# Performance work log

Hardware: AMD Instinct MI355X
Metric: run time of the kernel (lower is better)

## Reference

```python
import jax, jax.numpy as jnp
import numpy as np

HIDDEN = 2048
N_HEADS = 16
N_KV_HEADS = 8
HEAD_DIM = 128  # == head_dim_original, no padding needed
ROPE_THETA = 1000000.0
EPS = 1e-6
T_NOISE = 512
T_CTX = 1536
MAX_KV = 8192


def rms_norm(x, scale, eps=EPS):
    # normalize over last axis (head_dim), per-head like nnx.RMSNorm(head_dim)
    var = jnp.mean(x * x, axis=-1, keepdims=True)
    return x * jax.lax.rsqrt(var + eps) * scale


def apply_rope(x, positions, head_dim=HEAD_DIM, theta=ROPE_THETA):
    # x: (T, N, H), positions: (T,) int
    inv_freq = 1.0 / (theta ** (jnp.arange(0, head_dim, 2, dtype=jnp.float32) / head_dim))
    ang = positions.astype(jnp.float32)[:, None] * inv_freq  # (T, H/2)
    cos = jnp.cos(ang)[:, None, :]  # (T, 1, H/2)
    sin = jnp.sin(ang)[:, None, :]
    x1, x2 = jnp.split(x, 2, axis=-1)
    return jnp.concatenate([x1 * cos - x2 * sin, x2 * cos + x1 * sin], axis=-1).astype(x.dtype)


def setup_inputs() -> dict:
    key = jax.random.key(0)
    ks = jax.random.split(key, 10)
    s = 0.02
    return {
        "x_noise": jax.random.normal(ks[0], (T_NOISE, HIDDEN), jnp.float32),
        "target_hidden": jax.random.normal(ks[1], (T_CTX, HIDDEN), jnp.float32),
        "noise_positions": jnp.arange(T_NOISE, dtype=jnp.int32) + T_CTX,
        "ctx_positions": jnp.arange(T_CTX, dtype=jnp.int32),
        "kv_cache_k": jax.random.normal(ks[2], (1, N_HEADS, MAX_KV, HEAD_DIM), jnp.float32),
        "kv_cache_v": jax.random.normal(ks[3], (1, N_HEADS, MAX_KV, HEAD_DIM), jnp.float32),
        "cache_len": 2048,
        "wq": jax.random.normal(ks[4], (HIDDEN, N_HEADS, HEAD_DIM), jnp.float32) * s,
        "wk": jax.random.normal(ks[5], (HIDDEN, N_KV_HEADS, HEAD_DIM), jnp.float32) * s,
        "wv": jax.random.normal(ks[6], (HIDDEN, N_KV_HEADS, HEAD_DIM), jnp.float32) * s,
        "wo": jax.random.normal(ks[7], (N_HEADS, HEAD_DIM, HIDDEN), jnp.float32) * s,
        "q_scale": jnp.ones((HEAD_DIM,), jnp.float32) + jax.random.uniform(ks[8], (HEAD_DIM,), jnp.float32, -0.05, 0.05),
        "k_scale": jnp.ones((HEAD_DIM,), jnp.float32) + jax.random.uniform(ks[9], (HEAD_DIM,), jnp.float32, -0.05, 0.05),
    }


def reference(x_noise, target_hidden, noise_positions, ctx_positions, kv_cache_k,
              kv_cache_v, cache_len, wq, wk, wv, wo, q_scale, k_scale):
    num_kv_groups = N_HEADS // N_KV_HEADS
    t_noise = x_noise.shape[0]

    # 1. Q projection + RMSNorm + RoPE
    q = jnp.einsum('td,dnh->tnh', x_noise, wq)
    q = rms_norm(q, q_scale)
    q = apply_rope(q, noise_positions)

    # 2. K/V over [context, noise]
    x_new = jnp.concatenate([target_hidden, x_noise], axis=0)  # (T_new, D)
    k_new = jnp.einsum('td,dkh->tkh', x_new, wk)
    v_new = jnp.einsum('td,dkh->tkh', x_new, wv)
    k_new = rms_norm(k_new, k_scale)
    new_positions = jnp.concatenate([ctx_positions, noise_positions], axis=0)
    k_new = apply_rope(k_new, new_positions)

    # 3. GQA head repeat
    if num_kv_groups > 1:
        k_new = jnp.repeat(k_new, num_kv_groups, axis=1)
        v_new = jnp.repeat(v_new, num_kv_groups, axis=1)

    # 4. Scatter new K/V into cache at dynamic offset cache_len
    t_new = x_new.shape[0]
    k_new_4d = k_new.transpose(1, 0, 2)[None]  # (1, N, T_new, H)
    v_new_4d = v_new.transpose(1, 0, 2)[None]
    kv_cache_k = jax.lax.dynamic_update_slice(kv_cache_k, k_new_4d, (0, 0, cache_len, 0))
    kv_cache_v = jax.lax.dynamic_update_slice(kv_cache_v, v_new_4d, (0, 0, cache_len, 0))
    new_cache_len = cache_len + t_new
    max_kv = kv_cache_k.shape[2]

    # 5. Non-causal attention over valid cache (segment-id mask = valid length)
    q_4d = q.transpose(1, 0, 2)[None]  # (1, N, T_noise, H)
    sm_scale = HEAD_DIM ** -0.5
    scores = jnp.einsum('bnth,bnsh->bnts', q_4d, kv_cache_k) * sm_scale  # (1,N,Tq,S)
    valid = jnp.arange(max_kv) < new_cache_len  # (S,)
    scores = jnp.where(valid[None, None, None, :], scores, jnp.float32(-1e30))
    probs = jax.nn.softmax(scores, axis=-1)
    attn = jnp.einsum('bnts,bnsh->bnth', probs, kv_cache_v)
    attn = attn[0].transpose(1, 0, 2)  # (T_noise, N, H)

    output = jnp.einsum('tnh,nhd->td', attn, wo)
    return output, kv_cache_k, kv_cache_v
```

## Files before the change

### kernel.cpp

```cpp
#include <hip/hip_runtime.h>
#include <hip/hip_bf16.h>

#define HIDDEN 2048
#define NH 16
#define NKV 8
#define HD 128
#define TN 512
#define TC 1536
#define TNEW 2048
#define MAXKV 8192

using u16 = unsigned short;
using u32 = unsigned int;

typedef short short8 __attribute__((ext_vector_type(8)));
typedef float floatx4 __attribute__((ext_vector_type(4)));

__device__ __forceinline__ u16 f2bf(float f) {
  u32 u = __float_as_uint(f);
  u += 0x7FFFu + ((u >> 16) & 1u);
  return (u16)(u >> 16);
}

__device__ __forceinline__ uint4 pack8(const float* f) {
  uint4 r;
  r.x = (u32)f2bf(f[0]) | ((u32)f2bf(f[1]) << 16);
  r.y = (u32)f2bf(f[2]) | ((u32)f2bf(f[3]) << 16);
  r.z = (u32)f2bf(f[4]) | ((u32)f2bf(f[5]) << 16);
  r.w = (u32)f2bf(f[6]) | ((u32)f2bf(f[7]) << 16);
  return r;
}

__device__ __forceinline__ short8 ldfrag(const u16* p) {
  uint4 v = *(const uint4*)p;
  return __builtin_bit_cast(short8, v);
}

__device__ __forceinline__ void gload16(const void* g, void* l) {
  __builtin_amdgcn_global_load_lds(
      (const __attribute__((address_space(1))) u32*)g,
      (__attribute__((address_space(3))) u32*)l, 16, 0, 0);
}

__global__ __launch_bounds__(256) void cache_copy(
    const float4* __restrict__ inK, const float4* __restrict__ inV,
    float4* __restrict__ outK, float4* __restrict__ outV,
    const int* __restrict__ clp, u16* __restrict__ Kb, u16* __restrict__ VbT)
{
  const int cl = *clp;
  long long idx = (long long)blockIdx.x * 256 + threadIdx.x;
  const long long per = (long long)NH * MAXKV * (HD / 4);
  const float4* src; float4* dst; bool isv;
  long long r = idx;
  if (r < per) { src = inK; dst = outK; isv = false; }
  else { r -= per; src = inV; dst = outV; isv = true; }
  int row = (int)((r >> 5) & (MAXKV - 1));
  if (row >= cl && row < cl + TNEW) return;
  float4 v = src[r];
  dst[r] = v;
  if (row < cl) {
    if (!isv) {
      if (Kb) {
        uint2 p;
        p.x = (u32)f2bf(v.x) | ((u32)f2bf(v.y) << 16);
        p.y = (u32)f2bf(v.z) | ((u32)f2bf(v.w) << 16);
        *(uint2*)(Kb + (size_t)r * 4) = p;
      }
    } else if (VbT) {
      int head = (int)(r >> 18);
      int h0 = ((int)r & 31) * 4;
      size_t basev = ((size_t)head * HD + h0) * MAXKV + row;
      VbT[basev]             = f2bf(v.x);
      VbT[basev + MAXKV]     = f2bf(v.y);
      VbT[basev + 2 * MAXKV] = f2bf(v.z);
      VbT[basev + 3 * MAXKV] = f2bf(v.w);
    }
  }
}

__global__ __launch_bounds__(256) void gemm_bf16(
    const float* __restrict__ A0, int rows0, const float* __restrict__ A1,
    const float* __restrict__ B0, const float* __restrict__ B1, int Nhalf,
    float* __restrict__ C0, float* __restrict__ C1,
    int M, int N, int K, int ksteps)
{
  __shared__ u16 As[64 * 40];
  __shared__ u16 Bs[64 * 40];
  const int tid = threadIdx.x;
  const int lane = tid & 63;
  const int wave = tid >> 6;
  const int quad = lane >> 4;
  const int m16 = lane & 15;
  const int bm = blockIdx.y * 64;
  const int bn = blockIdx.x * 64;
  const int wm = (wave >> 1) * 32;
  const int wn = (wave & 1) * 32;
  const int z = blockIdx.z;
  const int kbase = z * ksteps * 32;

  const float* B = (bn < Nhalf) ? B0 : B1;
  float*       C = (bn < Nhalf) ? C0 : C1;
  const int n0 = (bn < Nhalf) ? bn : bn - Nhalf;
  const int strideN = (bn < Nhalf) ? Nhalf : (N - Nhalf);

  floatx4 acc[2][2];
#pragma unroll
  for (int i = 0; i < 2; i++)
#pragma unroll
    for (int j = 0; j < 2; j++)
#pragma unroll
      for (int r = 0; r < 4; r++) acc[i][j][r] = 0.0f;

  const int arow = tid >> 2, akg = (tid & 3) * 8;
  const int brow = tid >> 3, bng = (tid & 7) * 8;
  const int garow = bm + arow;
  const float* Ap = (garow < rows0) ? (A0 + (size_t)garow * K)
                                    : (A1 + (size_t)(garow - rows0) * K);

  for (int ks = 0; ks < ksteps; ks++) {
    const int k0 = kbase + ks * 32;
    if (k0 >= K) break;
    float av[8];
    *(float4*)(av)     = *(const float4*)(Ap + k0 + akg);
    *(float4*)(av + 4) = *(const float4*)(Ap + k0 + akg + 4);
    *(uint4*)&As[arow * 40 + akg] = pack8(av);

    float bv[8];
    const float* Bp = B + (size_t)(k0 + brow) * strideN + n0 + bng;
    *(float4*)(bv)     = *(const float4*)(Bp);
    *(float4*)(bv + 4) = *(const float4*)(Bp + 4);
#pragma unroll
    for (int j = 0; j < 8; j++) Bs[(bng + j) * 40 + brow] = f2bf(bv[j]);

    __syncthreads();

    short8 a0 = ldfrag(&As[(wm + m16) * 40 + quad * 8]);
    short8 a1 = ldfrag(&As[(wm + 16 + m16) * 40 + quad * 8]);
    short8 b0 = ldfrag(&Bs[(wn + m16) * 40 + quad * 8]);
    short8 b1 = ldfrag(&Bs[(wn + 16 + m16) * 40 + quad * 8]);
    acc[0][0] = __builtin_amdgcn_mfma_f32_16x16x32_bf16(a0, b0, acc[0][0], 0, 0, 0);
    acc[0][1] = __builtin_amdgcn_mfma_f32_16x16x32_bf16(a0, b1, acc[0][1], 0, 0, 0);
    acc[1][0] = __builtin_amdgcn_mfma_f32_16x16x32_bf16(a1, b0, acc[1][0], 0, 0, 0);
    acc[1][1] = __builtin_amdgcn_mfma_f32_16x16x32_bf16(a1, b1, acc[1][1], 0, 0, 0);

    __syncthreads();
  }

  const size_t zoff = (size_t)z * M * Nhalf;
#pragma unroll
  for (int mt = 0; mt < 2; mt++)
#pragma unroll
    for (int nt = 0; nt < 2; nt++)
#pragma unroll
      for (int r = 0; r < 4; r++) {
        int row = bm + wm + mt * 16 + quad * 4 + r;
        int col = wn + nt * 16 + m16;
        C[zoff + (size_t)row * strideN + n0 + col] = acc[mt][nt][r];
      }
}

__global__ __launch_bounds__(256) void reduce4(
    const float4* __restrict__ P, float4* __restrict__ C, int n4)
{
  int idx = blockIdx.x * 256 + threadIdx.x;
  if (idx >= n4) return;
  float4 a = P[idx], b = P[idx + n4], c = P[idx + 2 * n4], d = P[idx + 3 * n4];
  float4 r;
  r.x = (a.x + b.x) + (c.x + d.x);
  r.y = (a.y + b.y) + (c.y + d.y);
  r.z = (a.z + b.z) + (c.z + d.z);
  r.w = (a.w + b.w) + (c.w + d.w);
  C[idx] = r;
}

__global__ __launch_bounds__(64) void q_post_k(
    const float* __restrict__ qproj, const int* __restrict__ npos,
    const float* __restrict__ qscale, u16* __restrict__ qbf)
{
  const int t = blockIdx.x, n = blockIdx.y, i = threadIdx.x;
  const size_t base = (size_t)t * HIDDEN + n * HD;
  const float x1 = qproj[base + i];
  const float x2 = qproj[base + i + 64];
  float ss = x1 * x1 + x2 * x2;
#pragma unroll
  for (int m = 1; m < 64; m <<= 1) ss += __shfl_xor(ss, m, 64);
  const float rstd = rsqrtf(ss * (1.0f / HD) + 1e-6f);
  float y1 = x1 * rstd * qscale[i];
  float y2 = x2 * rstd * qscale[i + 64];
  const float pos = (float)npos[t];
  const float ang = pos * exp2f(-(float)i * (19.931568569324174f / 64.0f));
  const float c = cosf(ang), s = sinf(ang);
  const float sc = 0.08838834764831845f * 1.4426950408889634f;
  qbf[base + i]      = f2bf((y1 * c - y2 * s) * sc);
  qbf[base + i + 64] = f2bf((y2 * c + y1 * s) * sc);
}

__global__ __launch_bounds__(64) void k_post_k(
    const float* __restrict__ kproj, const int* __restrict__ ctxpos,
    const int* __restrict__ npos, const float* __restrict__ kscale,
    const int* __restrict__ clp, float* __restrict__ outK, u16* __restrict__ Kb)
{
  const int t = blockIdx.x, kh = blockIdx.y, i = threadIdx.x;
  const int cl = *clp;
  const size_t base = (size_t)t * (NKV * HD) + kh * HD;
  const float x1 = kproj[base + i];
  const float x2 = kproj[base + i + 64];
  float ss = x1 * x1 + x2 * x2;
#pragma unroll
  for (int m = 1; m < 64; m <<= 1) ss += __shfl_xor(ss, m, 64);
  const float rstd = rsqrtf(ss * (1.0f / HD) + 1e-6f);
  float y1 = x1 * rstd * kscale[i];
  float y2 = x2 * rstd * kscale[i + 64];
  const int posi = (t < TC) ? ctxpos[t] : npos[t - TC];
  const float ang = (float)posi * exp2f(-(float)i * (19.931568569324174f / 64.0f));
  const float c = cosf(ang), s = sinf(ang);
  const float o1 = y1 * c - y2 * s;
  const float o2 = y2 * c + y1 * s;
  const size_t row = (size_t)cl + t;
  const size_t b0 = ((size_t)(2 * kh) * MAXKV + row) * HD;
  const size_t b1 = ((size_t)(2 * kh + 1) * MAXKV + row) * HD;
  outK[b0 + i] = o1; outK[b0 + i + 64] = o2;
  outK[b1 + i] = o1; outK[b1 + i + 64] = o2;
  if (Kb) {
    const u16 s1 = f2bf(o1), s2 = f2bf(o2);
    Kb[b0 + i] = s1; Kb[b0 + i + 64] = s2;
    Kb[b1 + i] = s1; Kb[b1 + i + 64] = s2;
  }
}

__global__ __launch_bounds__(128) void v_post_k(
    const float* __restrict__ vproj, const int* __restrict__ clp,
    float* __restrict__ outV, u16* __restrict__ VbT)
{
  const int t = blockIdx.x, kh = blockIdx.y, h = threadIdx.x;
  const int cl = *clp;
  const float v = vproj[(size_t)t * (NKV * HD) + kh * HD + h];
  const size_t row = (size_t)cl + t;
  outV[((size_t)(2 * kh) * MAXKV + row) * HD + h] = v;
  outV[((size_t)(2 * kh + 1) * MAXKV + row) * HD + h] = v;
  if (VbT) {
    const u16 vb = f2bf(v);
    VbT[((size_t)(2 * kh) * HD + h) * MAXKV + row] = vb;
    VbT[((size_t)(2 * kh + 1) * HD + h) * MAXKV + row] = vb;
  }
}

__global__ __launch_bounds__(256) void attn_sh(
    const u16* __restrict__ qbf, const u16* __restrict__ Kb,
    const u16* __restrict__ VbT, const int* __restrict__ clp,
    float* __restrict__ Opart, float* __restrict__ Oml, int splits)
{
  __shared__ u16 Ks[2][32 * 128];
  __shared__ u16 Vt[2][128 * 32];
  __shared__ u16 Ps[4][16 * 40];

  const int tid = threadIdx.x;
  const int lane = tid & 63, wave = tid >> 6;
  const int quad = lane >> 4, m16 = lane & 15;

  const int lin = blockIdx.x;
  const int ppx = (NH * splits) >> 3;
  const int c = lin & 7;
  const int jj = lin >> 3;
  const int pair = c * ppx + (jj % ppx);
  const int x = jj / ppx;
  const int head = pair & (NH - 1);
  const int z = pair >> 4;

  const int qbase = x * 64 + wave * 16;
  const int Svalid = *clp + TNEW;
  const int ntiles = (Svalid + 31) >> 5;
  const int per = (ntiles + splits - 1) / splits;
  const int it0 = z * per;
  const int it1 = (ntiles < it0 + per) ? ntiles : (it0 + per);

  short8 qf[4];
#pragma unroll
  for (int kb = 0; kb < 4; kb++)
    qf[kb] = ldfrag(&qbf[((size_t)(qbase + m16) * NH + head) * HD + kb * 32 + quad * 8]);

  floatx4 O[8];
#pragma unroll
  for (int i = 0; i < 8; i++)
#pragma unroll
    for (int r = 0; r < 4; r++) O[i][r] = 0.0f;
  float mrow[4], lrow[4];
#pragma unroll
  for (int r = 0; r < 4; r++) { mrow[r] = -1e30f; lrow[r] = 0.0f; }

  const int krow = tid >> 4;
  const int ksrccol = ((tid & 15) * 16) ^ ((krow & 7) << 4);
  const char* Kbase = (const char*)(Kb + (size_t)head * MAXKV * HD);
  const int vh = tid >> 2;
  const int vs8 = (tid & 3) * 8;
  const char* Vbase = (const char*)(VbT + (size_t)head * HD * MAXKV);
  u16* myPs = &Ps[wave][0];
  const int kxor = (m16 & 7) << 4;
  const int wb = wave * 512;

  int b = 0;
  if (it0 < it1) {
    {
      const int s0 = it0 * 32;
      gload16(Kbase + ((size_t)(s0 + krow) << 8) + ksrccol,          &Ks[0][wb]);
      gload16(Kbase + ((size_t)(s0 + krow + 16) << 8) + ksrccol,     &Ks[0][2048 + wb]);
      gload16(Vbase + (((size_t)vh * MAXKV + s0 + vs8) << 1),        &Vt[0][wb]);
      gload16(Vbase + (((size_t)(vh + 64) * MAXKV + s0 + vs8) << 1), &Vt[0][2048 + wb]);
    }
    for (int it = it0; it < it1; ++it) {
      if (it + 1 < it1) {
        const int s1 = (it + 1) * 32;
        u16* KsN = &Ks[b ^ 1][0];
        u16* VtN = &Vt[b ^ 1][0];
        gload16(Kbase + ((size_t)(s1 + krow) << 8) + ksrccol,          KsN + wb);
        gload16(Kbase + ((size_t)(s1 + krow + 16) << 8) + ksrccol,     KsN + 2048 + wb);
        gload16(Vbase + (((size_t)vh * MAXKV + s1 + vs8) << 1),        VtN + wb);
        gload16(Vbase + (((size_t)(vh + 64) * MAXKV + s1 + vs8) << 1), VtN + 2048 + wb);
        asm volatile("s_waitcnt vmcnt(4) lgkmcnt(0)" ::: "memory");
      } else {
        asm volatile("s_waitcnt vmcnt(0) lgkmcnt(0)" ::: "memory");
      }
      __builtin_amdgcn_s_barrier();
      __builtin_amdgcn_sched_barrier(0);

      const u16* KsB = &Ks[b][0];
      const u16* VtB = &Vt[b][0];
      const int s0 = it * 32;

      floatx4 sc[2];
#pragma unroll
      for (int st = 0; st < 2; st++) {
        floatx4 a;
#pragma unroll
        for (int r = 0; r < 4; r++) a[r] = 0.0f;
        const int rofs = (st * 16 + m16) * 128;
#pragma unroll
        for (int kb = 0; kb < 4; kb++) {
          short8 kf = ldfrag(&KsB[rofs + (((kb * 64 + quad * 16) ^ kxor) >> 1)]);
          a = __builtin_amdgcn_mfma_f32_16x16x32_bf16(qf[kb], kf, a, 0, 0, 0);
        }
        const int scol = s0 + st * 16 + m16;
        if (scol >= Svalid) {
#pragma unroll
          for (int r = 0; r < 4; r++) a[r] = -1e30f;
        }
        sc[st] = a;
      }

      float alpha[4];
#pragma unroll
      for (int r = 0; r < 4; r++) {
        float mx = fmaxf(sc[0][r], sc[1][r]);
        mx = fmaxf(mx, __shfl_xor(mx, 1, 64));
        mx = fmaxf(mx, __shfl_xor(mx, 2, 64));
        mx = fmaxf(mx, __shfl_xor(mx, 4, 64));
        mx = fmaxf(mx, __shfl_xor(mx, 8, 64));
        const float mn = fmaxf(mrow[r], mx);
        alpha[r] = exp2f(mrow[r] - mn);
        const float p0 = exp2f(sc[0][r] - mn);
        const float p1 = exp2f(sc[1][r] - mn);
        sc[0][r] = p0; sc[1][r] = p1;
        float rs = p0 + p1;
        rs += __shfl_xor(rs, 1, 64);
        rs += __shfl_xor(rs, 2, 64);
        rs += __shfl_xor(rs, 4, 64);
        rs += __shfl_xor(rs, 8, 64);
        lrow[r] = lrow[r] * alpha[r] + rs;
        mrow[r] = mn;
      }
#pragma unroll
      for (int hb = 0; hb < 8; hb++)
#pragma unroll
        for (int r = 0; r < 4; r++) O[hb][r] *= alpha[r];

#pragma unroll
      for (int st = 0; st < 2; st++)
#pragma unroll
        for (int r = 0; r < 4; r++)
          myPs[(quad * 4 + r) * 40 + st * 16 + m16] = f2bf(sc[st][r]);
      short8 pfr = ldfrag(&myPs[m16 * 40 + quad * 8]);
#pragma unroll
      for (int hb = 0; hb < 8; hb++) {
        short8 vf = ldfrag(&VtB[(hb * 16 + m16) * 32 + quad * 8]);
        O[hb] = __builtin_amdgcn_mfma_f32_16x16x32_bf16(pfr, vf, O[hb], 0, 0, 0);
      }

      asm volatile("s_waitcnt lgkmcnt(0)" ::: "memory");
      __builtin_amdgcn_s_barrier();
      __builtin_amdgcn_sched_barrier(0);
      b ^= 1;
    }
  }

  const size_t zbase = (size_t)z * TN * NH;
  const int trow = qbase + quad * 4;
#pragma unroll
  for (int hb = 0; hb < 8; hb++)
#pragma unroll
    for (int r = 0; r < 4; r++)
      Opart[(zbase + (size_t)(trow + r) * NH + head) * HD + hb * 16 + m16] = O[hb][r];
  if (m16 == 0) {
#pragma unroll
    for (int r = 0; r < 4; r++) {
      Oml[(zbase + (size_t)(trow + r) * NH + head) * 2 + 0] = mrow[r];
      Oml[(zbase + (size_t)(trow + r) * NH + head) * 2 + 1] = lrow[r];
    }
  }
}

__global__ __launch_bounds__(256) void attn_k(
    const u16* __restrict__ qbf, const float* __restrict__ outK,
    const float* __restrict__ outV, const int* __restrict__ clp,
    float* __restrict__ Opart, float* __restrict__ Oml)
{
  __shared__ u16 Ksl[32 * 136];
  __shared__ u16 Vtl[128 * 40];
  __shared__ u16 Psl[4 * 16 * 40];
  const int tid = threadIdx.x;
  const int lane = tid & 63, wave = tid >> 6;
  const int quad = lane >> 4, m16 = lane & 15;
  const int head = blockIdx.y;
  const int qbase = blockIdx.x * 64 + wave * 16;
  const int z = blockIdx.z, splits = gridDim.z;
  const int Svalid = *clp + TNEW;
  const int ntiles = (Svalid + 31) >> 5;
  const int per = (ntiles + splits - 1) / splits;
  const int it0 = z * per;
  const int it1 = min(ntiles, it0 + per);

  short8 qf[4];
#pragma unroll
  for (int kb = 0; kb < 4; kb++)
    qf[kb] = ldfrag(&qbf[((size_t)(qbase + m16) * NH + head) * HD + kb * 32 + quad * 8]);

  floatx4 O[8];
#pragma unroll
  for (int i = 0; i < 8; i++)
#pragma unroll
    for (int r = 0; r < 4; r++) O[i][r] = 0.0f;
  float mrow[4], lrow[4];
#pragma unroll
  for (int r = 0; r < 4; r++) { mrow[r] = -1e30f; lrow[r] = 0.0f; }

  const int sstage = tid >> 3;
  const int hg = (tid & 7) * 16;

  for (int it = it0; it < it1; it++) {
    const int s0 = it * 32;
    {
      int srow = s0 + sstage; if (srow > MAXKV - 1) srow = MAXKV - 1;
      const float* kp = outK + ((size_t)head * MAXKV + srow) * HD + hg;
      float tv[16];
      *(float4*)(tv)      = *(const float4*)(kp);
      *(float4*)(tv + 4)  = *(const float4*)(kp + 4);
      *(float4*)(tv + 8)  = *(const float4*)(kp + 8);
      *(float4*)(tv + 12) = *(const float4*)(kp + 12);
      *(uint4*)&Ksl[sstage * 136 + hg]     = pack8(tv);
      *(uint4*)&Ksl[sstage * 136 + hg + 8] = pack8(tv + 8);
      const float* vp = outV + ((size_t)head * MAXKV + srow) * HD + hg;
      float vv[16];
      *(float4*)(vv)      = *(const float4*)(vp);
      *(float4*)(vv + 4)  = *(const float4*)(vp + 4);
      *(float4*)(vv + 8)  = *(const float4*)(vp + 8);
      *(float4*)(vv + 12) = *(const float4*)(vp + 12);
#pragma unroll
      for (int j = 0; j < 16; j++) Vtl[(hg + j) * 40 + sstage] = f2bf(vv[j]);
    }
    __syncthreads();

    floatx4 sc[2];
#pragma unroll
    for (int st = 0; st < 2; st++) {
      floatx4 a;
#pragma unroll
      for (int r = 0; r < 4; r++) a[r] = 0.0f;
#pragma unroll
      for (int kb = 0; kb < 4; kb++) {
        short8 kf = ldfrag(&Ksl[(st * 16 + m16) * 136 + kb * 32 + quad * 8]);
        a = __builtin_amdgcn_mfma_f32_16x16x32_bf16(qf[kb], kf, a, 0, 0, 0);
      }
      const int scol = s0 + st * 16 + m16;
      if (scol >= Svalid) {
#pragma unroll
        for (int r = 0; r < 4; r++) a[r] = -1e30f;
      }
      sc[st] = a;
    }

    float alpha[4];
#pragma unroll
    for (int r = 0; r < 4; r++) {
      float mx = fmaxf(sc[0][r], sc[1][r]);
      mx = fmaxf(mx, __shfl_xor(mx, 1, 64));
      mx = fmaxf(mx, __shfl_xor(mx, 2, 64));
      mx = fmaxf(mx, __shfl_xor(mx, 4, 64));
      mx = fmaxf(mx, __shfl_xor(mx, 8, 64));
      const float mn = fmaxf(mrow[r], mx);
      alpha[r] = exp2f(mrow[r] - mn);
      const float p0 = exp2f(sc[0][r] - mn);
      const float p1 = exp2f(sc[1][r] - mn);
      sc[0][r] = p0; sc[1][r] = p1;
      float rs = p0 + p1;
      rs += __shfl_xor(rs, 1, 64);
      rs += __shfl_xor(rs, 2, 64);
      rs += __shfl_xor(rs, 4, 64);
      rs += __shfl_xor(rs, 8, 64);
      lrow[r] = lrow[r] * alpha[r] + rs;
      mrow[r] = mn;
    }
#pragma unroll
    for (int hb = 0; hb < 8; hb++)
#pragma unroll
      for (int r = 0; r < 4; r++) O[hb][r] *= alpha[r];

    u16* myPs = &Psl[wave * 640];
#pragma unroll
    for (int st = 0; st < 2; st++)
#pragma unroll
      for (int r = 0; r < 4; r++)
        myPs[(quad * 4 + r) * 40 + st * 16 + m16] = f2bf(sc[st][r]);
    short8 pf = ldfrag(&myPs[m16 * 40 + quad * 8]);
#pragma unroll
    for (int hb = 0; hb < 8; hb++) {
      short8 vf = ldfrag(&Vtl[(hb * 16 + m16) * 40 + quad * 8]);
      O[hb] = __builtin_amdgcn_mfma_f32_16x16x32_bf16(pf, vf, O[hb], 0, 0, 0);
    }
    __syncthreads();
  }

  const size_t zbase = (size_t)z * TN * NH;
  const int trow = qbase + quad * 4;
#pragma unroll
  for (int hb = 0; hb < 8; hb++)
#pragma unroll
    for (int r = 0; r < 4; r++)
      Opart[(zbase + (size_t)(trow + r) * NH + head) * HD + hb * 16 + m16] = O[hb][r];
  if (m16 == 0) {
#pragma unroll
    for (int r = 0; r < 4; r++) {
      Oml[(zbase + (size_t)(trow + r) * NH + head) * 2 + 0] = mrow[r];
      Oml[(zbase + (size_t)(trow + r) * NH + head) * 2 + 1] = lrow[r];
    }
  }
}

__global__ __launch_bounds__(128) void attn_combine(
    const float* __restrict__ Opart, const float* __restrict__ Oml,
    float* __restrict__ attnb, int splits)
{
  const int pair = blockIdx.x;
  const int h = threadIdx.x;
  float M = -1e30f;
  for (int zz = 0; zz < splits; zz++)
    M = fmaxf(M, Oml[((size_t)zz * TN * NH + pair) * 2]);
  float l = 0.0f, o = 0.0f;
  for (int zz = 0; zz < splits; zz++) {
    const float mi = Oml[((size_t)zz * TN * NH + pair) * 2];
    const float li = Oml[((size_t)zz * TN * NH + pair) * 2 + 1];
    const float w = exp2f(mi - M);
    l += li * w;
    o += Opart[((size_t)zz * TN * NH + pair) * HD + h] * w;
  }
  attnb[(size_t)pair * HD + h] = o / l;
}

extern "C" void kernel_launch(void* const* d_in, const int* in_sizes, int n_in,
                              void* d_out, int out_size, void* d_ws, size_t ws_size,
                              hipStream_t stream) {
  const float* x_noise       = (const float*)d_in[0];
  const float* target_hidden = (const float*)d_in[1];
  const int*   noise_pos     = (const int*)d_in[2];
  const int*   ctx_pos       = (const int*)d_in[3];
  const float* inK           = (const float*)d_in[4];
  const float* inV           = (const float*)d_in[5];
  const int*   cache_len     = (const int*)d_in[6];
  const float* wq            = (const float*)d_in[7];
  const float* wk            = (const float*)d_in[8];
  const float* wv            = (const float*)d_in[9];
  const float* wo            = (const float*)d_in[10];
  const float* q_scale       = (const float*)d_in[11];
  const float* k_scale       = (const float*)d_in[12];

  float* out0 = (float*)d_out;
  float* outK = out0 + (size_t)TN * HIDDEN;
  float* outV = outK + (size_t)NH * MAXKV * HD;

  size_t off = 0;
  auto walloc = [&](size_t bytes) -> void* {
    void* p = (char*)d_ws + off;
    off += (bytes + 255) & ~(size_t)255;
    return p;
  };
  u16*   qbf   = (u16*)walloc((size_t)TN * HIDDEN * 2);
  float* attnb = (float*)walloc((size_t)TN * HIDDEN * 4);
  float* qproj = (float*)walloc((size_t)TN * HIDDEN * 4);
  float* kproj = (float*)walloc((size_t)TNEW * NKV * HD * 4);
  float* vproj = (float*)walloc((size_t)TNEW * NKV * HD * 4);

  const size_t PER_SPLIT = (size_t)TN * NH * HD * 4 + (size_t)TN * NH * 8;
  const size_t SHB = (size_t)NH * MAXKV * HD * sizeof(u16);
  const size_t GPART = (size_t)4 * TN * HIDDEN * 4;
  auto maxsz = [](size_t a, size_t b) { return a > b ? a : b; };

  size_t avail = (ws_size > off) ? ws_size - off : 0;
  u16 *Kb = nullptr, *VbT = nullptr;
  int asplits = 0;
  if (avail >= 2 * SHB + maxsz(8 * PER_SPLIT, GPART))       asplits = 8;
  else if (avail >= 2 * SHB + maxsz(4 * PER_SPLIT, GPART))  asplits = 4;
  const bool shadow = (asplits > 0);
  if (shadow) {
    Kb  = (u16*)walloc(SHB);
    VbT = (u16*)walloc(SHB);
  }

  float* scratch = (float*)((char*)d_ws + off);
  const size_t avail2 = (ws_size > off) ? ws_size - off : 0;
  if (!shadow) {
    asplits = 2;
    if (avail2 >= 8 * PER_SPLIT) asplits = 8;
    else if (avail2 >= 4 * PER_SPLIT) asplits = 4;
  }
  float* Opart = scratch;
  float* Oml   = Opart + (size_t)asplits * TN * NH * HD;
  const bool ksplit = (avail2 >= GPART);
  float* gpart = scratch;

  cache_copy<<<dim3(32768), dim3(256), 0, stream>>>(
      (const float4*)inK, (const float4*)inV, (float4*)outK, (float4*)outV,
      cache_len, Kb, VbT);

  if (ksplit) {
    gemm_bf16<<<dim3(HIDDEN / 64, TN / 64, 4), dim3(256), 0, stream>>>(
        x_noise, TN, x_noise, wq, wq, HIDDEN, gpart, gpart, TN, HIDDEN, HIDDEN, 16);
    reduce4<<<dim3((TN * HIDDEN / 4 + 255) / 256), dim3(256), 0, stream>>>(
        (const float4*)gpart, (float4*)qproj, TN * HIDDEN / 4);
  } else {
    gemm_bf16<<<dim3(HIDDEN / 64, TN / 64, 1), dim3(256), 0, stream>>>(
        x_noise, TN, x_noise, wq, wq, HIDDEN, qproj, qproj, TN, HIDDEN, HIDDEN, 64);
  }

  gemm_bf16<<<dim3(2 * NKV * HD / 64, TNEW / 64, 1), dim3(256), 0, stream>>>(
      target_hidden, TC, x_noise, wk, wv, NKV * HD, kproj, vproj,
      TNEW, 2 * NKV * HD, HIDDEN, 64);

  q_post_k<<<dim3(TN, NH), dim3(64), 0, stream>>>(qproj, noise_pos, q_scale, qbf);
  k_post_k<<<dim3(TNEW, NKV), dim3(64), 0, stream>>>(
      kproj, ctx_pos, noise_pos, k_scale, cache_len, outK, Kb);
  v_post_k<<<dim3(TNEW, NKV), dim3(128), 0, stream>>>(vproj, cache_len, outV, VbT);

  if (shadow) {
    attn_sh<<<dim3((TN / 64) * NH * asplits), dim3(256), 0, stream>>>(
        qbf, Kb, VbT, cache_len, Opart, Oml, asplits);
  } else {
    attn_k<<<dim3(TN / 64, NH, asplits), dim3(256), 0, stream>>>(
        qbf, outK, outV, cache_len, Opart, Oml);
  }
  attn_combine<<<dim3(TN * NH), dim3(128), 0, stream>>>(Opart, Oml, attnb, asplits);

  if (ksplit) {
    gemm_bf16<<<dim3(HIDDEN / 64, TN / 64, 4), dim3(256), 0, stream>>>(
        attnb, TN, attnb, wo, wo, HIDDEN, gpart, gpart, TN, HIDDEN, HIDDEN, 16);
    reduce4<<<dim3((TN * HIDDEN / 4 + 255) / 256), dim3(256), 0, stream>>>(
        (const float4*)gpart, (float4*)out0, TN * HIDDEN / 4);
  } else {
    gemm_bf16<<<dim3(HIDDEN / 64, TN / 64, 1), dim3(256), 0, stream>>>(
        attnb, TN, attnb, wo, wo, HIDDEN, out0, out0, TN, HIDDEN, HIDDEN, 64);
  }
}
```

Before: 565.6 us.

## Pre-convert activations and weights to bf16 and use 128x128 double-buffered GEMM

Result: faster. 528.9 us (-6.5%).

```diff
diff --git a/kernel.cpp b/kernel.cpp
--- a/kernel.cpp
+++ b/kernel.cpp
@@ -40,6 +40,45 @@
   __builtin_amdgcn_global_load_lds(
       (const __attribute__((address_space(1))) u32*)g,
       (__attribute__((address_space(3))) u32*)l, 16, 0, 0);
+}
+
+__global__ __launch_bounds__(256) void conv_bf16(
+    const float4* __restrict__ in, uint2* __restrict__ out, int n4)
+{
+  int idx = blockIdx.x * 256 + threadIdx.x;
+  if (idx >= n4) return;
+  float4 v = in[idx];
+  uint2 r;
+  r.x = (u32)f2bf(v.x) | ((u32)f2bf(v.y) << 16);
+  r.y = (u32)f2bf(v.z) | ((u32)f2bf(v.w) << 16);
+  out[idx] = r;
+}
+
+__global__ __launch_bounds__(256) void transpose_bf16(
+    const float* __restrict__ w, u16* __restrict__ wT, int K, int N)
+{
+  __shared__ float t[64][65];
+  const int bk = blockIdx.y * 64, bn = blockIdx.x * 64;
+  const int tid = threadIdx.x;
+  const int r = tid >> 4, c4 = (tid & 15) * 4;
+#pragma unroll
+  for (int rr = 0; rr < 4; rr++) {
+    float4 v = *(const float4*)(w + (size_t)(bk + rr * 16 + r) * N + bn + c4);
+    t[rr * 16 + r][c4 + 0] = v.x;
+    t[rr * 16 + r][c4 + 1] = v.y;
+    t[rr * 16 + r][c4 + 2] = v.z;
+    t[rr * 16 + r][c4 + 3] = v.w;
+  }
+  __syncthreads();
+  const int n = tid >> 2, k16 = (tid & 3) * 16;
+  u32 wbuf[8];
+#pragma unroll
+  for (int jj = 0; jj < 8; jj++) {
+    float lo = t[k16 + 2 * jj][n], hi = t[k16 + 2 * jj + 1][n];
+    wbuf[jj] = (u32)f2bf(lo) | ((u32)f2bf(hi) << 16);
+  }
+  *(uint4*)(&wT[(size_t)(bn + n) * K + bk + k16])     = *(uint4*)(wbuf);
+  *(uint4*)(&wT[(size_t)(bn + n) * K + bk + k16 + 8]) = *(uint4*)(wbuf + 4);
 }
 
 __global__ __launch_bounds__(256) void cache_copy(
@@ -78,6 +117,109 @@
   }
 }
 
+__global__ __launch_bounds__(256) void gemm_v2(
+    const u16* __restrict__ A0, int rows0, const u16* __restrict__ A1,
+    const u16* __restrict__ B0, const u16* __restrict__ B1, int Nhalf,
+    float* __restrict__ C0, float* __restrict__ C1,
+    int M, int N, int K, int ksteps)
+{
+  __shared__ u16 As[2][128 * 32];
+  __shared__ u16 Bs[2][128 * 32];
+  const int tid = threadIdx.x;
+  const int lane = tid & 63, wave = tid >> 6;
+  const int quad = lane >> 4, m16 = lane & 15;
+
+  const int gx = gridDim.x, gy = gridDim.y;
+  int bx = blockIdx.x, by = blockIdx.y;
+  if (((gx & 3) == 0) && ((gy & 1) == 0)) {
+    const int lin = bx + gx * by;
+    const int c = lin & 7, j = lin >> 3;
+    const int sw = gx >> 2, sh = gy >> 1;
+    bx = (c & 3) * sw + j % sw;
+    by = (c >> 2) * sh + j / sw;
+  }
+  const int bm = by * 128, bn = bx * 128;
+  const int wm = (wave >> 1) * 64, wn = (wave & 1) * 64;
+  const int z = blockIdx.z;
+  const int kbase = z * ksteps * 32;
+
+  const u16* B = (bn < Nhalf) ? B0 : B1;
+  float*     C = (bn < Nhalf) ? C0 : C1;
+  const int n0 = (bn < Nhalf) ? bn : bn - Nhalf;
+  const int strideN = (bn < Nhalf) ? Nhalf : (N - Nhalf);
+
+  floatx4 acc[4][4];
+#pragma unroll
+  for (int i = 0; i < 4; i++)
+#pragma unroll
+    for (int j = 0; j < 4; j++)
+#pragma unroll
+      for (int r = 0; r < 4; r++) acc[i][j][r] = 0.0f;
+
+  const int srow = tid >> 2;
+  const int sk = (tid & 3) * 8;
+  const int ar0 = bm + srow, ar1 = bm + srow + 64;
+  const u16* Arow0 = (ar0 < rows0) ? (A0 + (size_t)ar0 * K)
+                                   : (A1 + (size_t)(ar0 - rows0) * K);
+  const u16* Arow1 = (ar1 < rows0) ? (A0 + (size_t)ar1 * K)
+                                   : (A1 + (size_t)(ar1 - rows0) * K);
+  const u16* Brow0 = B + (size_t)(n0 + srow) * K;
+  const u16* Brow1 = B + (size_t)(n0 + srow + 64) * K;
+  const int wb = wave * 512;
+
+  {
+    const int k0 = kbase;
+    gload16(Arow0 + k0 + sk, &As[0][wb]);
+    gload16(Arow1 + k0 + sk, &As[0][2048 + wb]);
+    gload16(Brow0 + k0 + sk, &Bs[0][wb]);
+    gload16(Brow1 + k0 + sk, &Bs[0][2048 + wb]);
+  }
+  int b = 0;
+  for (int ks = 0; ks < ksteps; ks++) {
+    if (ks + 1 < ksteps) {
+      const int k1 = kbase + (ks + 1) * 32;
+      gload16(Arow0 + k1 + sk, &As[b ^ 1][wb]);
+      gload16(Arow1 + k1 + sk, &As[b ^ 1][2048 + wb]);
+      gload16(Brow0 + k1 + sk, &Bs[b ^ 1][wb]);
+      gload16(Brow1 + k1 + sk, &Bs[b ^ 1][2048 + wb]);
+      asm volatile("s_waitcnt vmcnt(4)" ::: "memory");
+    } else {
+      asm volatile("s_waitcnt vmcnt(0)" ::: "memory");
+    }
+    __builtin_amdgcn_s_barrier();
+    __builtin_amdgcn_sched_barrier(0);
+
+    short8 af[4], bfr[4];
+#pragma unroll
+    for (int i = 0; i < 4; i++) {
+      af[i]  = ldfrag(&As[b][(wm + i * 16 + m16) * 32 + quad * 8]);
+      bfr[i] = ldfrag(&Bs[b][(wn + i * 16 + m16) * 32 + quad * 8]);
+    }
+#pragma unroll
+    for (int i = 0; i < 4; i++)
+#pragma unroll
+      for (int j = 0; j < 4; j++)
+        acc[i][j] = __builtin_amdgcn_mfma_f32_16x16x32_bf16(af[i], bfr[j], acc[i][j], 0, 0, 0);
+
+    asm volatile("s_waitcnt lgkmcnt(0)" ::: "memory");
+    __builtin_amdgcn_s_barrier();
+    __builtin_amdgcn_sched_barrier(0);
+    b ^= 1;
+  }
+
+  const size_t zoff = (size_t)z * M * Nhalf;
+#pragma unroll
+  for (int i = 0; i < 4; i++)
+#pragma unroll
+    for (int j = 0; j < 4; j++)
+#pragma unroll
+      for (int r = 0; r < 4; r++) {
+        int row = bm + wm + i * 16 + quad * 4 + r;
+        int col = wn + j * 16 + m16;
+        C[zoff + (size_t)row * strideN + n0 + col] = acc[i][j][r];
+      }
+}
+
 __global__ __launch_bounds__(256) void gemm_bf16(
     const float* __restrict__ A0, int rows0, const float* __restrict__ A1,
     const float* __restrict__ B0, const float* __restrict__ B1, int Nhalf,
@@ -546,7 +688,7 @@
 
 __global__ __launch_bounds__(128) void attn_combine(
     const float* __restrict__ Opart, const float* __restrict__ Oml,
-    float* __restrict__ attnb, int splits)
+    float* __restrict__ attnb, u16* __restrict__ attnbf, int splits)
 {
   const int pair = blockIdx.x;
   const int h = threadIdx.x;
@@ -561,7 +703,9 @@
     l += li * w;
     o += Opart[((size_t)zz * TN * NH + pair) * HD + h] * w;
   }
-  attnb[(size_t)pair * HD + h] = o / l;
+  const float res = o / l;
+  attnb[(size_t)pair * HD + h] = res;
+  if (attnbf) attnbf[(size_t)pair * HD + h] = f2bf(res);
 }
 
 extern "C" void kernel_launch(void* const* d_in, const int* in_sizes, int n_in,
@@ -591,23 +735,41 @@
     off += (bytes + 255) & ~(size_t)255;
     return p;
   };
-  u16*   qbf   = (u16*)walloc((size_t)TN * HIDDEN * 2);
-  float* attnb = (float*)walloc((size_t)TN * HIDDEN * 4);
-  float* qproj = (float*)walloc((size_t)TN * HIDDEN * 4);
-  float* kproj = (float*)walloc((size_t)TNEW * NKV * HD * 4);
-  float* vproj = (float*)walloc((size_t)TNEW * NKV * HD * 4);
+  u16*   qbf    = (u16*)walloc((size_t)TN * HIDDEN * 2);
+  float* attnb  = (float*)walloc((size_t)TN * HIDDEN * 4);
+  u16*   attnbf = (u16*)walloc((size_t)TN * HIDDEN * 2);
+  float* qproj  = (float*)walloc((size_t)TN * HIDDEN * 4);
+  float* kproj  = (float*)walloc((size_t)TNEW * NKV * HD * 4);
+  float* vproj  = (float*)walloc((size_t)TNEW * NKV * HD * 4);
 
   const size_t PER_SPLIT = (size_t)TN * NH * HD * 4 + (size_t)TN * NH * 8;
-  const size_t SHB = (size_t)NH * MAXKV * HD * sizeof(u16);
+  const size_t SHB   = (size_t)NH * MAXKV * HD * sizeof(u16);
   const size_t GPART = (size_t)4 * TN * HIDDEN * 4;
+  const size_t CONVB = ((size_t)TN * HIDDEN + (size_t)TC * HIDDEN) * 2
+                     + ((size_t)HIDDEN * HIDDEN * 2
+                      + (size_t)HIDDEN * (NKV * HD) * 2) * 2;
   auto maxsz = [](size_t a, size_t b) { return a > b ? a : b; };
 
   size_t avail = (ws_size > off) ? ws_size - off : 0;
+  bool conv = false;
+  int asplits = 0;
+  if (avail >= CONVB + 2 * SHB + maxsz(8 * PER_SPLIT, GPART))      { conv = true; asplits = 8; }
+  else if (avail >= CONVB + 2 * SHB + maxsz(4 * PER_SPLIT, GPART)) { conv = true; asplits = 4; }
+  else if (avail >= 2 * SHB + maxsz(8 * PER_SPLIT, GPART))         { asplits = 8; }
+  else if (avail >= 2 * SHB + maxsz(4 * PER_SPLIT, GPART))         { asplits = 4; }
+  const bool shadow = (asplits > 0);
+
+  u16 *xbf = nullptr, *thbf = nullptr, *wqT = nullptr, *wkT = nullptr,
+      *wvT = nullptr, *woT = nullptr;
+  if (conv) {
+    xbf  = (u16*)walloc((size_t)TN * HIDDEN * 2);
+    thbf = (u16*)walloc((size_t)TC * HIDDEN * 2);
+    wqT  = (u16*)walloc((size_t)HIDDEN * HIDDEN * 2);
+    wkT  = (u16*)walloc((size_t)HIDDEN * (NKV * HD) * 2);
+    wvT  = (u16*)walloc((size_t)HIDDEN * (NKV * HD) * 2);
+    woT  = (u16*)walloc((size_t)HIDDEN * HIDDEN * 2);
+  }
   u16 *Kb = nullptr, *VbT = nullptr;
-  int asplits = 0;
-  if (avail >= 2 * SHB + maxsz(8 * PER_SPLIT, GPART))       asplits = 8;
-  else if (avail >= 2 * SHB + maxsz(4 * PER_SPLIT, GPART))  asplits = 4;
-  const bool shadow = (asplits > 0);
   if (shadow) {
     Kb  = (u16*)walloc(SHB);
     VbT = (u16*)walloc(SHB);
@@ -625,11 +787,34 @@
   const bool ksplit = (avail2 >= GPART);
   float* gpart = scratch;
 
+  if (conv) {
+    conv_bf16<<<dim3((TN * HIDDEN / 4 + 255) / 256), dim3(256), 0, stream>>>(
+        (const float4*)x_noise, (uint2*)xbf, TN * HIDDEN / 4);
+    conv_bf16<<<dim3((TC * HIDDEN / 4 + 255) / 256), dim3(256), 0, stream>>>(
+        (const float4*)target_hidden, (uint2*)thbf, TC * HIDDEN / 4);
+    transpose_bf16<<<dim3(HIDDEN / 64, HIDDEN / 64), dim3(256), 0, stream>>>(
+        wq, wqT, HIDDEN, HIDDEN);
+    transpose_bf16<<<dim3(NKV * HD / 64, HIDDEN / 64), dim3(256), 0, stream>>>(
+        wk, wkT, HIDDEN, NKV * HD);
+    transpose_bf16<<<dim3(NKV * HD / 64, HIDDEN / 64), dim3(256), 0, stream>>>(
+        wv, wvT, HIDDEN, NKV * HD);
+    transpose_bf16<<<dim3(HIDDEN / 64, HIDDEN / 64), dim3(256), 0, stream>>>(
+        wo, woT, NH * HD, HIDDEN);
+  }
+
   cache_copy<<<dim3(32768), dim3(256), 0, stream>>>(
       (const float4*)inK, (const float4*)inV, (float4*)outK, (float4*)outV,
       cache_len, Kb, VbT);
 
-  if (ksplit) {
+  if (conv && ksplit) {
+    gemm_v2<<<dim3(HIDDEN / 128, TN / 128, 4), dim3(256), 0, stream>>>(
+        xbf, TN, xbf, wqT, wqT, HIDDEN, gpart, gpart, TN, HIDDEN, HIDDEN, 16);
+    reduce4<<<dim3((TN * HIDDEN / 4 + 255) / 256), dim3(256), 0, stream>>>(
+        (const float4*)gpart, (float4*)qproj, TN * HIDDEN / 4);
+  } else if (conv) {
+    gemm_v2<<<dim3(HIDDEN / 128, TN / 128, 1), dim3(256), 0, stream>>>(
+        xbf, TN, xbf, wqT, wqT, HIDDEN, qproj, qproj, TN, HIDDEN, HIDDEN, 64);
+  } else if (ksplit) {
     gemm_bf16<<<dim3(HIDDEN / 64, TN / 64, 4), dim3(256), 0, stream>>>(
         x_noise, TN, x_noise, wq, wq, HIDDEN, gpart, gpart, TN, HIDDEN, HIDDEN, 16);
     reduce4<<<dim3((TN * HIDDEN / 4 + 255) / 256), dim3(256), 0, stream>>>(
@@ -639,9 +824,15 @@
         x_noise, TN, x_noise, wq, wq, HIDDEN, qproj, qproj, TN, HIDDEN, HIDDEN, 64);
   }
 
-  gemm_bf16<<<dim3(2 * NKV * HD / 64, TNEW / 64, 1), dim3(256), 0, stream>>>(
-      target_hidden, TC, x_noise, wk, wv, NKV * HD, kproj, vproj,
-      TNEW, 2 * NKV * HD, HIDDEN, 64);
+  if (conv) {
+    gemm_v2<<<dim3(2 * NKV * HD / 128, TNEW / 128, 1), dim3(256), 0, stream>>>(
+        thbf, TC, xbf, wkT, wvT, NKV * HD, kproj, vproj,
+        TNEW, 2 * NKV * HD, HIDDEN, 64);
+  } else {
+    gemm_bf16<<<dim3(2 * NKV * HD / 64, TNEW / 64, 1), dim3(256), 0, stream>>>(
+        target_hidden, TC, x_noise, wk, wv, NKV * HD, kproj, vproj,
+        TNEW, 2 * NKV * HD, HIDDEN, 64);
+  }
 
   q_post_k<<<dim3(TN, NH), dim3(64), 0, stream>>>(qproj, noise_pos, q_scale, qbf);
   k_post_k<<<dim3(TNEW, NKV), dim3(64), 0, stream>>>(
@@ -655,9 +846,18 @@
     attn_k<<<dim3(TN / 64, NH, asplits), dim3(256), 0, stream>>>(
         qbf, outK, outV, cache_len, Opart, Oml);
   }
-  attn_combine<<<dim3(TN * NH), dim3(128), 0, stream>>>(Opart, Oml, attnb, asplits);
-
-  if (ksplit) {
+  attn_combine<<<dim3(TN * NH), dim3(128), 0, stream>>>(
+      Opart, Oml, attnb, conv ? attnbf : nullptr, asplits);
+
+  if (conv && ksplit) {
+    gemm_v2<<<dim3(HIDDEN / 128, TN / 128, 4), dim3(256), 0, stream>>>(
+        attnbf, TN, attnbf, woT, woT, HIDDEN, gpart, gpart, TN, HIDDEN, HIDDEN, 16);
+    reduce4<<<dim3((TN * HIDDEN / 4 + 255) / 256), dim3(256), 0, stream>>>(
+        (const float4*)gpart, (float4*)out0, TN * HIDDEN / 4);
+  } else if (conv) {
+    gemm_v2<<<dim3(HIDDEN / 128, TN / 128, 1), dim3(256), 0, stream>>>(
+        attnbf, TN, attnbf, woT, woT, HIDDEN, out0, out0, TN, HIDDEN, HIDDEN, 64);
+  } else if (ksplit) {
     gemm_bf16<<<dim3(HIDDEN / 64, TN / 64, 4), dim3(256), 0, stream>>>(
         attnb, TN, attnb, wo, wo, HIDDEN, gpart, gpart, TN, HIDDEN, HIDDEN, 16);
     reduce4<<<dim3((TN * HIDDEN / 4 + 255) / 256), dim3(256), 0, stream>>>(
```
